# Optimization experiments

Hardware: AMD Instinct MI355X
Metric: run time of the kernel (lower is better)

The kernel has to match this reference:

```python
import jax, jax.numpy as jnp
import numpy as np


def setup_inputs() -> dict:
    key = jax.random.key(0)
    kq, kk, kv = jax.random.split(key, 3)
    B, S, H, HK, D = 2, 2048, 32, 8, 128
    q = jax.random.normal(kq, (B, S, H, D), dtype=jnp.float32)
    k = jax.random.normal(kk, (B, S, HK, D), dtype=jnp.float32)
    v = jax.random.normal(kv, (B, S, HK, D), dtype=jnp.float32)
    return {"q": q, "k": k, "v": v}


def reference(q, k, v):
    # Causal grouped-query attention (the math vLLM's paged attention computes
    # for a full prefill where the KV cache holds exactly this sequence).
    B, S, H, D = q.shape
    HK = k.shape[2]
    G = H // HK  # query heads per kv head
    scale = jnp.asarray(D, q.dtype) ** -0.5
    qg = q.reshape(B, S, HK, G, D)
    # scores: [B, HK, G, S(q), S(k)]
    scores = jnp.einsum("bshgd,bthd->bhgst", qg, k) * scale
    causal = jnp.tril(jnp.ones((S, S), dtype=bool))  # [Sq, Sk]
    scores = jnp.where(causal, scores, jnp.finfo(scores.dtype).min)
    probs = jax.nn.softmax(scores, axis=-1)
    out = jnp.einsum("bhgst,bthd->bshgd", probs, v)  # [B, S, HK, G, D]
    return out.reshape(B, S, H * D)
```

## Files before the change

kernel.cpp:

```cpp
#include <hip/hip_runtime.h>
#include <hip/hip_bf16.h>

typedef __attribute__((ext_vector_type(8))) short short8;
typedef __attribute__((ext_vector_type(4))) short short4v;
typedef __attribute__((ext_vector_type(4))) float f32x4;
typedef __attribute__((ext_vector_type(16))) float f32x16;

#define MFMA32(a,b,c) __builtin_amdgcn_mfma_f32_32x32x16_bf16(a,b,c,0,0,0)

static __device__ __forceinline__ short f2bf(float f){
    union{float f;unsigned u;}x; x.f=f;
    unsigned r=(x.u+0x7FFFu+((x.u>>16)&1u))>>16;
    return (short)r;
}

static __device__ __forceinline__ unsigned pkbf(float lo, float hi){
    unsigned r;
    asm("v_cvt_pk_bf16_f32 %0, %1, %2" : "=v"(r) : "v"(lo), "v"(hi));
    return r;
}

static __device__ __forceinline__ void gl_lds16(const void* g, void* l){
    __builtin_amdgcn_global_load_lds(
        (const __attribute__((address_space(1))) unsigned int*)g,
        (__attribute__((address_space(3))) unsigned int*)l, 16, 0, 0);
}

static __device__ __forceinline__ short8 pfrag(int hi,
        float e0,float e1,float e2,float e3,
        float e4,float e5,float e6,float e7){
    unsigned a01 = pkbf(e0,e1), a23 = pkbf(e2,e3);
    unsigned a45 = pkbf(e4,e5), a67 = pkbf(e6,e7);
    unsigned b01 = __shfl_xor(a01, 32);
    unsigned b23 = __shfl_xor(a23, 32);
    unsigned b45 = __shfl_xor(a45, 32);
    unsigned b67 = __shfl_xor(a67, 32);
    union{ unsigned u[4]; short8 s; } w;
    w.u[0] = hi ? b45 : a01;
    w.u[1] = hi ? b67 : a23;
    w.u[2] = hi ? a45 : b01;
    w.u[3] = hi ? a67 : b23;
    return w.s;
}

constexpr int S_=2048, H_=32, HK_=8, D_=128;
constexpr int KVBLK=64;

__global__ __launch_bounds__(256) void prep(const float* __restrict__ k, const float* __restrict__ v,
                                            short* __restrict__ kb, short* __restrict__ vt){
    __shared__ short tile[64*65];
    int bid = blockIdx.x;
    if (bid < 4096){
        int t = bid*256 + threadIdx.x;
        int e = t*4;
        int d  = e & 127;
        int hk = (e>>7) & 7;
        int s  = (e>>10) & 2047;
        int b  = e>>21;
        f32x4 x = *(const f32x4*)(k + ((size_t)((b*S_+s)*HK_+hk))*D_ + d);
        short4v o;
        o[0]=f2bf(x[0]); o[1]=f2bf(x[1]); o[2]=f2bf(x[2]); o[3]=f2bf(x[3]);
        *(short4v*)(kb + ((size_t)((b*HK_+hk)*S_+s))*D_ + d) = o;
    } else {
        bid -= 4096;
        int d0 = (bid & 1)*64;
        int s0 = ((bid>>1) & 31)*64;
        int hk = (bid>>6) & 7;
        int b  = bid>>9;
        int tid = threadIdx.x;
        #pragma unroll
        for(int i=0;i<4;i++){
            int idx = i*1024 + tid*4;
            int r = idx>>6, c = idx&63;
            f32x4 x = *(const f32x4*)(v + ((size_t)((b*S_+s0+r)*HK_+hk))*D_ + d0 + c);
            tile[(c+0)*65 + r] = f2bf(x[0]);
            tile[(c+1)*65 + r] = f2bf(x[1]);
            tile[(c+2)*65 + r] = f2bf(x[2]);
            tile[(c+3)*65 + r] = f2bf(x[3]);
        }
        __syncthreads();
        #pragma unroll
        for(int i=0;i<4;i++){
            int idx = i*1024 + tid*4;
            int dr = idx>>6, c = idx&63;
            short4v o;
            o[0]=tile[dr*65+c]; o[1]=tile[dr*65+c+1]; o[2]=tile[dr*65+c+2]; o[3]=tile[dr*65+c+3];
            *(short4v*)(vt + ((size_t)((b*HK_+hk)*D_ + d0+dr))*S_ + s0 + c) = o;
        }
    }
}

__global__ __launch_bounds__(256,2) void attn_fwd(
    const float* __restrict__ q, const short* __restrict__ kb,
    const short* __restrict__ vtb, float* __restrict__ out)
{
    __shared__ __align__(16) unsigned char kls[2][KVBLK*D_*2];
    __shared__ __align__(16) unsigned char vls[2][D_*KVBLK*2];

    const int bid  = blockIdx.x;
    const int wg   = (bid & 7)*64 + (bid >> 3);
    const int kvg  = wg >> 5;
    const int b    = kvg >> 3;
    const int hk   = kvg & 7;
    const int rr_  = wg & 31;
    const int h    = hk*4 + (rr_ >> 3);
    const int pair = rr_ & 7;

    const int tid  = threadIdx.x;
    const int wave = tid >> 6;
    const int ln   = tid & 31;
    const int hi   = (tid >> 5) & 1;

    const float qscale = 0.08838834764831845f * 1.4426950408889634f;

    const short* kt_base = kb  + (size_t)(b*HK_+hk)*S_*D_;
    const short* vt_base = vtb + (size_t)(b*HK_+hk)*D_*S_;

    auto STAGE = [&](int bufi, int kvt){
        const char* kg = (const char*)(kt_base + (size_t)kvt*KVBLK*D_);
        #pragma unroll
        for(int i=0;i<4;i++){
            int p = (i*256 + tid)*16;
            int src = p ^ (((p>>8)&7)<<4);
            gl_lds16(kg + src, &kls[bufi][p]);
        }
        const char* vg = (const char*)vt_base + (size_t)kvt*KVBLK*2;
        #pragma unroll
        for(int i=0;i<4;i++){
            int p = (i*256 + tid)*16;
            int d = p>>7;
            int src = (p&127) ^ ((d&7)<<4);
            gl_lds16(vg + (size_t)d*(S_*2) + src, &vls[bufi][p]);
        }
    };

    int cur = 0;
    STAGE(0, 0);
    __syncthreads();

    for(int phase=0; phase<2; ++phase){
        const int c      = phase ? pair : 15-pair;
        const int nkv    = 2*c + 2;
        const int kvmaxw = 2*c + (wave >> 1);
        const int qg     = c*128 + wave*32 + ln;

        short8 qf[8];
        {
            const float* qp = q + ((size_t)(b*S_ + qg)*H_ + h)*D_;
            #pragma unroll
            for(int kk=0;kk<8;kk++){
                int d0 = kk*16 + hi*8;
                f32x4 a = *(const f32x4*)(qp + d0);
                f32x4 cc= *(const f32x4*)(qp + d0 + 4);
                union{ unsigned u[4]; short8 s; } w;
                w.u[0]=pkbf(a[0]*qscale, a[1]*qscale);
                w.u[1]=pkbf(a[2]*qscale, a[3]*qscale);
                w.u[2]=pkbf(cc[0]*qscale, cc[1]*qscale);
                w.u[3]=pkbf(cc[2]*qscale, cc[3]*qscale);
                qf[kk]=w.s;
            }
        }

        f32x16 oac[4];
        #pragma unroll
        for(int dt=0;dt<4;dt++) oac[dt] = (f32x16)0.f;
        float l = 0.f;

        for(int kvt=0; kvt<nkv; ++kvt){
            int nxt = (kvt+1 < nkv) ? (kvt+1) : (phase==0 ? 0 : -1);
            if (nxt >= 0) STAGE(cur^1, nxt);

            if (kvt <= kvmaxw){
                const int kv0 = kvt*64;
                f32x16 sa0=(f32x16)0.f, sa1=(f32x16)0.f;
                const int sz = (ln&7)<<4;
                __builtin_amdgcn_s_setprio(1);
                #pragma unroll
                for(int kk=0;kk<8;kk++){
                    int cb = kk*32 + hi*16;
                    short8 k0 = *(const short8*)&kls[cur][(ln*256 + cb) ^ sz];
                    short8 k1 = *(const short8*)&kls[cur][((ln+32)*256 + cb) ^ sz];
                    sa0 = MFMA32(k0, qf[kk], sa0);
                    sa1 = MFMA32(k1, qf[kk], sa1);
                }
                __builtin_amdgcn_s_setprio(0);
                if (kv0 + 63 > c*128 + wave*32){
                    #pragma unroll
                    for(int r=0;r<16;r++){
                        int kvl = (r&3) + 8*(r>>2) + 4*hi;
                        if (kv0 + kvl      > qg) sa0[r] = -1e30f;
                        if (kv0 + 32 + kvl > qg) sa1[r] = -1e30f;
                    }
                }
                float ps0=0.f, ps1=0.f, ps2=0.f, ps3=0.f;
                #pragma unroll
                for(int r=0;r<16;r+=4){
                    sa0[r+0]=__builtin_amdgcn_exp2f(sa0[r+0]); ps0+=sa0[r+0];
                    sa0[r+1]=__builtin_amdgcn_exp2f(sa0[r+1]); ps1+=sa0[r+1];
                    sa0[r+2]=__builtin_amdgcn_exp2f(sa0[r+2]); ps2+=sa0[r+2];
                    sa0[r+3]=__builtin_amdgcn_exp2f(sa0[r+3]); ps3+=sa0[r+3];
                }
                #pragma unroll
                for(int r=0;r<16;r+=4){
                    sa1[r+0]=__builtin_amdgcn_exp2f(sa1[r+0]); ps0+=sa1[r+0];
                    sa1[r+1]=__builtin_amdgcn_exp2f(sa1[r+1]); ps1+=sa1[r+1];
                    sa1[r+2]=__builtin_amdgcn_exp2f(sa1[r+2]); ps2+=sa1[r+2];
                    sa1[r+3]=__builtin_amdgcn_exp2f(sa1[r+3]); ps3+=sa1[r+3];
                }
                float ps = (ps0+ps1)+(ps2+ps3);
                l += ps + __shfl_xor(ps, 32);
                short8 pa0 = pfrag(hi, sa0[0],sa0[1],sa0[2], sa0[3], sa0[4], sa0[5], sa0[6], sa0[7]);
                short8 pa1 = pfrag(hi, sa0[8],sa0[9],sa0[10],sa0[11],sa0[12],sa0[13],sa0[14],sa0[15]);
                short8 pa2 = pfrag(hi, sa1[0],sa1[1],sa1[2], sa1[3], sa1[4], sa1[5], sa1[6], sa1[7]);
                short8 pa3 = pfrag(hi, sa1[8],sa1[9],sa1[10],sa1[11],sa1[12],sa1[13],sa1[14],sa1[15]);
                __builtin_amdgcn_s_setprio(1);
                #pragma unroll
                for(int dt=0;dt<4;dt++){
                    int rb = (dt*32 + ln)*128;
                    short8 v0 = *(const short8*)&vls[cur][(rb +   0 + hi*16) ^ sz];
                    oac[dt] = MFMA32(v0, pa0, oac[dt]);
                    short8 v1 = *(const short8*)&vls[cur][(rb +  32 + hi*16) ^ sz];
                    oac[dt] = MFMA32(v1, pa1, oac[dt]);
                    short8 v2 = *(const short8*)&vls[cur][(rb +  64 + hi*16) ^ sz];
                    oac[dt] = MFMA32(v2, pa2, oac[dt]);
                    short8 v3 = *(const short8*)&vls[cur][(rb +  96 + hi*16) ^ sz];
                    oac[dt] = MFMA32(v3, pa3, oac[dt]);
                }
                __builtin_amdgcn_s_setprio(0);
            }
            __syncthreads();
            cur ^= 1;
        }

        float rinv = 1.0f / l;
        float* op = out + ((size_t)(b*S_ + qg)*H_ + h)*D_;
        #pragma unroll
        for(int dt=0;dt<4;dt++){
            #pragma unroll
            for(int rr=0;rr<4;rr++){
                f32x4 o4;
                o4[0]=oac[dt][rr*4+0]*rinv;
                o4[1]=oac[dt][rr*4+1]*rinv;
                o4[2]=oac[dt][rr*4+2]*rinv;
                o4[3]=oac[dt][rr*4+3]*rinv;
                *(f32x4*)(op + dt*32 + rr*8 + hi*4) = o4;
            }
        }
    }
}

extern "C" void kernel_launch(void* const* d_in, const int* in_sizes, int n_in,
                              void* d_out, int out_size, void* d_ws, size_t ws_size,
                              hipStream_t stream) {
    const float* q = (const float*)d_in[0];
    const float* k = (const float*)d_in[1];
    const float* v = (const float*)d_in[2];
    float* out = (float*)d_out;

    short* kb = (short*)d_ws;
    short* vt = (short*)((char*)d_ws + (size_t)2*HK_*S_*D_*2);

    prep<<<dim3(4096+1024), dim3(256), 0, stream>>>(k, v, kb, vt);
    attn_fwd<<<dim3(512), dim3(256), 0, stream>>>(q, kb, vt, out);
}
```

Before: 111.5 us.

## Software-pipeline QK of next KV tile with softmax and PV of previous

Splits K and V staging into separate async LDS loads and restructures the KV loop into a two-stage software pipeline. The QK^T MFMAs for tile t+1 are issued alongside the exp/softmax and PV MFMAs for tile t, using two sets of score accumulators. The goal is to hide the dependency latency between QK, softmax and PV, and to stage V one step later than K. The cost is extra live score registers, which may reduce occupancy, a fresh prologue per phase instead of the previous cross-phase prefetch, and an added barrier at the end of each phase.

```diff
diff --git a/kernel.cpp b/kernel.cpp
--- a/kernel.cpp
+++ b/kernel.cpp
@@ -116,33 +116,36 @@
     const short* kt_base = kb  + (size_t)(b*HK_+hk)*S_*D_;
     const short* vt_base = vtb + (size_t)(b*HK_+hk)*D_*S_;
 
-    auto STAGE = [&](int bufi, int kvt){
+    auto STAGE_K = [&](int kvt){
         const char* kg = (const char*)(kt_base + (size_t)kvt*KVBLK*D_);
+        unsigned char* kd = kls[kvt&1];
         #pragma unroll
         for(int i=0;i<4;i++){
             int p = (i*256 + tid)*16;
             int src = p ^ (((p>>8)&7)<<4);
-            gl_lds16(kg + src, &kls[bufi][p]);
-        }
+            gl_lds16(kg + src, kd + p);
+        }
+    };
+    auto STAGE_V = [&](int kvt){
         const char* vg = (const char*)vt_base + (size_t)kvt*KVBLK*2;
+        unsigned char* vd = vls[kvt&1];
         #pragma unroll
         for(int i=0;i<4;i++){
             int p = (i*256 + tid)*16;
             int d = p>>7;
             int src = (p&127) ^ ((d&7)<<4);
-            gl_lds16(vg + (size_t)d*(S_*2) + src, &vls[bufi][p]);
+            gl_lds16(vg + (size_t)d*(S_*2) + src, vd + p);
         }
     };
 
-    int cur = 0;
-    STAGE(0, 0);
-    __syncthreads();
+    const int sz = (ln&7)<<4;
 
     for(int phase=0; phase<2; ++phase){
         const int c      = phase ? pair : 15-pair;
         const int nkv    = 2*c + 2;
         const int kvmaxw = 2*c + (wave >> 1);
         const int qg     = c*128 + wave*32 + ln;
+        const int qw0    = c*128 + wave*32;
 
         short8 qf[8];
         {
@@ -166,71 +169,99 @@
         for(int dt=0;dt<4;dt++) oac[dt] = (f32x16)0.f;
         float l = 0.f;
 
-        for(int kvt=0; kvt<nkv; ++kvt){
-            int nxt = (kvt+1 < nkv) ? (kvt+1) : (phase==0 ? 0 : -1);
-            if (nxt >= 0) STAGE(cur^1, nxt);
-
-            if (kvt <= kvmaxw){
-                const int kv0 = kvt*64;
-                f32x16 sa0=(f32x16)0.f, sa1=(f32x16)0.f;
-                const int sz = (ln&7)<<4;
-                __builtin_amdgcn_s_setprio(1);
+        auto QK = [&](int kvt, f32x16 &s0, f32x16 &s1){
+            const int cur = kvt & 1;
+            s0 = (f32x16)0.f; s1 = (f32x16)0.f;
+            __builtin_amdgcn_s_setprio(1);
+            #pragma unroll
+            for(int kk=0;kk<8;kk++){
+                int cb = kk*32 + hi*16;
+                short8 k0 = *(const short8*)&kls[cur][(ln*256 + cb) ^ sz];
+                short8 k1 = *(const short8*)&kls[cur][((ln+32)*256 + cb) ^ sz];
+                s0 = MFMA32(k0, qf[kk], s0);
+                s1 = MFMA32(k1, qf[kk], s1);
+            }
+            __builtin_amdgcn_s_setprio(0);
+            const int kv0 = kvt*64;
+            if (kv0 + 63 > qw0){
                 #pragma unroll
-                for(int kk=0;kk<8;kk++){
-                    int cb = kk*32 + hi*16;
-                    short8 k0 = *(const short8*)&kls[cur][(ln*256 + cb) ^ sz];
-                    short8 k1 = *(const short8*)&kls[cur][((ln+32)*256 + cb) ^ sz];
-                    sa0 = MFMA32(k0, qf[kk], sa0);
-                    sa1 = MFMA32(k1, qf[kk], sa1);
+                for(int r=0;r<16;r++){
+                    int kvl = (r&3) + 8*(r>>2) + 4*hi;
+                    if (kv0 + kvl      > qg) s0[r] = -1e30f;
+                    if (kv0 + 32 + kvl > qg) s1[r] = -1e30f;
                 }
-                __builtin_amdgcn_s_setprio(0);
-                if (kv0 + 63 > c*128 + wave*32){
-                    #pragma unroll
-                    for(int r=0;r<16;r++){
-                        int kvl = (r&3) + 8*(r>>2) + 4*hi;
-                        if (kv0 + kvl      > qg) sa0[r] = -1e30f;
-                        if (kv0 + 32 + kvl > qg) sa1[r] = -1e30f;
-                    }
-                }
-                float ps0=0.f, ps1=0.f, ps2=0.f, ps3=0.f;
-                #pragma unroll
-                for(int r=0;r<16;r+=4){
-                    sa0[r+0]=__builtin_amdgcn_exp2f(sa0[r+0]); ps0+=sa0[r+0];
-                    sa0[r+1]=__builtin_amdgcn_exp2f(sa0[r+1]); ps1+=sa0[r+1];
-                    sa0[r+2]=__builtin_amdgcn_exp2f(sa0[r+2]); ps2+=sa0[r+2];
-                    sa0[r+3]=__builtin_amdgcn_exp2f(sa0[r+3]); ps3+=sa0[r+3];
-                }
-                #pragma unroll
-                for(int r=0;r<16;r+=4){
-                    sa1[r+0]=__builtin_amdgcn_exp2f(sa1[r+0]); ps0+=sa1[r+0];
-                    sa1[r+1]=__builtin_amdgcn_exp2f(sa1[r+1]); ps1+=sa1[r+1];
-                    sa1[r+2]=__builtin_amdgcn_exp2f(sa1[r+2]); ps2+=sa1[r+2];
-                    sa1[r+3]=__builtin_amdgcn_exp2f(sa1[r+3]); ps3+=sa1[r+3];
-                }
-                float ps = (ps0+ps1)+(ps2+ps3);
-                l += ps + __shfl_xor(ps, 32);
-                short8 pa0 = pfrag(hi, sa0[0],sa0[1],sa0[2], sa0[3], sa0[4], sa0[5], sa0[6], sa0[7]);
-                short8 pa1 = pfrag(hi, sa0[8],sa0[9],sa0[10],sa0[11],sa0[12],sa0[13],sa0[14],sa0[15]);
-                short8 pa2 = pfrag(hi, sa1[0],sa1[1],sa1[2], sa1[3], sa1[4], sa1[5], sa1[6], sa1[7]);
-                short8 pa3 = pfrag(hi, sa1[8],sa1[9],sa1[10],sa1[11],sa1[12],sa1[13],sa1[14],sa1[15]);
-                __builtin_amdgcn_s_setprio(1);
-                #pragma unroll
-                for(int dt=0;dt<4;dt++){
-                    int rb = (dt*32 + ln)*128;
-                    short8 v0 = *(const short8*)&vls[cur][(rb +   0 + hi*16) ^ sz];
-                    oac[dt] = MFMA32(v0, pa0, oac[dt]);
-                    short8 v1 = *(const short8*)&vls[cur][(rb +  32 + hi*16) ^ sz];
-                    oac[dt] = MFMA32(v1, pa1, oac[dt]);
-                    short8 v2 = *(const short8*)&vls[cur][(rb +  64 + hi*16) ^ sz];
-                    oac[dt] = MFMA32(v2, pa2, oac[dt]);
-                    short8 v3 = *(const short8*)&vls[cur][(rb +  96 + hi*16) ^ sz];
-                    oac[dt] = MFMA32(v3, pa3, oac[dt]);
-                }
-                __builtin_amdgcn_s_setprio(0);
-            }
+            }
+        };
+
+        auto SMPV = [&](int kvt, f32x16 &s0, f32x16 &s1){
+            const int cur = kvt & 1;
+            float ps0=0.f, ps1=0.f, ps2=0.f, ps3=0.f;
+            #pragma unroll
+            for(int r=0;r<16;r+=4){
+                s0[r+0]=__builtin_amdgcn_exp2f(s0[r+0]); ps0+=s0[r+0];
+                s0[r+1]=__builtin_amdgcn_exp2f(s0[r+1]); ps1+=s0[r+1];
+                s0[r+2]=__builtin_amdgcn_exp2f(s0[r+2]); ps2+=s0[r+2];
+                s0[r+3]=__builtin_amdgcn_exp2f(s0[r+3]); ps3+=s0[r+3];
+            }
+            #pragma unroll
+            for(int r=0;r<16;r+=4){
+                s1[r+0]=__builtin_amdgcn_exp2f(s1[r+0]); ps0+=s1[r+0];
+                s1[r+1]=__builtin_amdgcn_exp2f(s1[r+1]); ps1+=s1[r+1];
+                s1[r+2]=__builtin_amdgcn_exp2f(s1[r+2]); ps2+=s1[r+2];
+                s1[r+3]=__builtin_amdgcn_exp2f(s1[r+3]); ps3+=s1[r+3];
+            }
+            float ps = (ps0+ps1)+(ps2+ps3);
+            l += ps + __shfl_xor(ps, 32);
+            short8 pa0 = pfrag(hi, s0[0],s0[1],s0[2], s0[3], s0[4], s0[5], s0[6], s0[7]);
+            short8 pa1 = pfrag(hi, s0[8],s0[9],s0[10],s0[11],s0[12],s0[13],s0[14],s0[15]);
+            short8 pa2 = pfrag(hi, s1[0],s1[1],s1[2], s1[3], s1[4], s1[5], s1[6], s1[7]);
+            short8 pa3 = pfrag(hi, s1[8],s1[9],s1[10],s1[11],s1[12],s1[13],s1[14],s1[15]);
+            __builtin_amdgcn_s_setprio(1);
+            #pragma unroll
+            for(int dt=0;dt<4;dt++){
+                int rb = (dt*32 + ln)*128;
+                short8 v0 = *(const short8*)&vls[cur][(rb +   0 + hi*16) ^ sz];
+                oac[dt] = MFMA32(v0, pa0, oac[dt]);
+                short8 v1 = *(const short8*)&vls[cur][(rb +  32 + hi*16) ^ sz];
+                oac[dt] = MFMA32(v1, pa1, oac[dt]);
+                short8 v2 = *(const short8*)&vls[cur][(rb +  64 + hi*16) ^ sz];
+                oac[dt] = MFMA32(v2, pa2, oac[dt]);
+                short8 v3 = *(const short8*)&vls[cur][(rb +  96 + hi*16) ^ sz];
+                oac[dt] = MFMA32(v3, pa3, oac[dt]);
+            }
+            __builtin_amdgcn_s_setprio(0);
+        };
+
+        f32x16 sA0, sA1, sB0, sB1;
+
+        STAGE_K(0);
+        __syncthreads();
+        QK(0, sA0, sA1);
+        STAGE_K(1);
+        STAGE_V(0);
+
+        __syncthreads();
+        if (1 <= kvmaxw) QK(1, sB0, sB1);
+        SMPV(0, sA0, sA1);
+        if (2 < nkv) STAGE_K(2);
+        STAGE_V(1);
+
+        for(int tt=2; tt+1<nkv; tt+=2){
             __syncthreads();
-            cur ^= 1;
-        }
+            if (tt <= kvmaxw) QK(tt, sA0, sA1);
+            SMPV(tt-1, sB0, sB1);
+            if (tt+1 < nkv) STAGE_K(tt+1);
+            STAGE_V(tt);
+
+            __syncthreads();
+            if (tt+1 <= kvmaxw) QK(tt+1, sB0, sB1);
+            SMPV(tt, sA0, sA1);
+            if (tt+2 < nkv) STAGE_K(tt+2);
+            STAGE_V(tt+1);
+        }
+
+        __syncthreads();
+        if (nkv-1 <= kvmaxw) SMPV(nkv-1, sB0, sB1);
 
         float rinv = 1.0f / l;
         float* op = out + ((size_t)(b*S_ + qg)*H_ + h)*D_;
@@ -246,6 +277,7 @@
                 *(f32x4*)(op + dt*32 + rr*8 + hi*4) = o4;
             }
         }
+        __syncthreads();
     }
 }
 
```

New measurement: 170.0 us. 52.5% more time.
